# Performance work log

Hardware: AMD Instinct MI355X
Metric: run time of the kernel (lower is better)

The kernel has to match this reference:

```python
import jax, jax.numpy as jnp
import numpy as np

N = 100000   # n_node
D = 100      # emb_size
K = 100      # K1 (channel 0 cluster count)
L = 3        # layers
NNZ = 1600000  # sparse adjacency nnz (avg degree 16)


def _l2norm(x):
    # F.normalize(x, dim=-1, p=2) with eps=1e-12
    return x / jnp.maximum(jnp.linalg.norm(x, axis=-1, keepdims=True), 1e-12)


def setup_inputs() -> dict:
    key = jax.random.key(0)
    ks = jax.random.split(key, 8)
    s = 1.0 / np.sqrt(D)  # module's uniform(-stdv, stdv) init
    embedding = jax.random.normal(ks[0], (N, D), jnp.float32)
    adj = jax.random.uniform(ks[1], (N,), jnp.float32) + 0.01  # per-node positive weights
    edge_rows = jax.random.randint(ks[2], (NNZ,), 0, N, jnp.int32)
    edge_cols = jax.random.randint(ks[3], (NNZ,), 0, N, jnp.int32)
    edge_vals = jax.random.uniform(ks[4], (NNZ,), jnp.float32)
    W_item = jax.random.uniform(ks[5], (L, D, D), jnp.float32, -s, s)
    W_i1 = jax.random.uniform(ks[6], (D, D), jnp.float32, -s, s)
    W_i2 = jax.random.uniform(ks[7], (D, K), jnp.float32, -s, s)
    return {"embedding": embedding, "adj": adj, "edge_vals": edge_vals,
            "W_item": W_item, "W_i1": W_i1, "W_i2": W_i2,
            "edge_rows": edge_rows, "edge_cols": edge_cols}


def reference(embedding, adj, edge_vals, W_item, W_i1, W_i2, edge_rows, edge_cols):
    # ItemConv.forward for one channel (channel=0), adjacency as COO sparse [N,N]
    def spmm(x):  # torch.sparse.mm(adjacency, x)
        return jax.ops.segment_sum(edge_vals[:, None] * x[edge_cols], edge_rows,
                                   num_segments=N)

    x = embedding
    final = [x]
    finalh = []
    for i in range(L):
        x = x @ W_item[i]                       # Linear(D, D, bias=False)
        x = spmm(x)                             # [N, D]
        H1 = jax.nn.relu(x @ W_i1 + x)          # residual + ReLU
        H1 = jax.nn.softmax(H1 @ W_i2, axis=1)  # [N, K] soft cluster assignment
        h = H1.T * adj[None, :]                 # [K, N]
        h = h / jnp.sum(h, axis=0)              # column-normalize over clusters
        h = h @ x                               # [K, D] cluster aggregates
        h = H1 @ h                              # [N, D] redistribute to nodes
        x = h + x                               # residual
        final.append(_l2norm(x))
        finalh.append(_l2norm(h))
    item_embeddings = sum(final) / (L + 1)
    hs = sum(finalh) / L
    return item_embeddings, hs
```

## Files before the change

### kernel.cpp

```cpp
#include <hip/hip_runtime.h>
#include <hip/hip_bf16.h>

#define D 100
#define XS 128

typedef __hip_bfloat16 bf16;
typedef __attribute__((ext_vector_type(8))) short bf16x8;
typedef __attribute__((ext_vector_type(4))) float f32x4;

__device__ __forceinline__ float ldf(const void* p, long long i, int f32) {
    return f32 ? ((const float*)p)[i] : __bfloat162float(((const bf16*)p)[i]);
}

__device__ __forceinline__ float b2f(unsigned short u) {
    return __uint_as_float(((unsigned int)u) << 16);
}

__device__ __forceinline__ unsigned short f2bu(float x) {
    union { bf16 b; unsigned short u; } cv;
    cv.b = __float2bfloat16(x);
    return cv.u;
}

__global__ void detectk(const void* __restrict__ emb, int* __restrict__ flag)
{
    const unsigned short* u = (const unsigned short*)emb;
    __shared__ int cnt;
    if (threadIdx.x == 0) cnt = 0;
    __syncthreads();
    int good = 0;
    for (int i = threadIdx.x; i < 512; i += 256) {
        int e = (u[i] >> 7) & 0xFF;
        if (e >= 118 && e <= 137) good++;
    }
    atomicAdd(&cnt, good);
    __syncthreads();
    if (threadIdx.x == 0) *flag = (cnt >= 410) ? 0 : 1;
}


__global__ void wprep(const void* __restrict__ wi, const void* __restrict__ w1,
    const void* __restrict__ w2, const int* __restrict__ flag,
    bf16* __restrict__ wh, bf16* __restrict__ wl)
{
    int i = blockIdx.x * 256 + threadIdx.x;
    if (i >= 5 * 112 * 128) return;
    int m = i / (112 * 128), rem = i - m * (112 * 128);
    int c = rem / 128, k = rem - c * 128;
    float w = 0.f;
    if (c < D && k < D) {
        int f = *flag;
        long long si = (long long)k * D + c;
        if (m < 3)       w = ldf(wi, m * 10000 + si, f);
        else if (m == 3) w = ldf(w1, si, f);
        else             w = ldf(w2, si, f);
    }
    bf16 hb = __float2bfloat16(w);
    wh[i] = hb;
    wl[i] = __float2bfloat16(w - __bfloat162float(hb));
}


__global__ void hsm_conv(const float* __restrict__ hsm, bf16* __restrict__ hh,
    bf16* __restrict__ hl)
{
    int i = blockIdx.x * 256 + threadIdx.x;
    if (i >= 112 * 128) return;
    int c = i / 128, k = i - c * 128;
    float w = (c < D && k < D) ? hsm[k * D + c] : 0.f;
    bf16 hb = __float2bfloat16(w);
    hh[i] = hb;
    hl[i] = __float2bfloat16(w - __bfloat162float(hb));
}

__global__ void initk(const void* __restrict__ emb, const int* __restrict__ flag,
    bf16* __restrict__ x, float* __restrict__ o0, float* __restrict__ o1, int n)
{
    long long i = (long long)blockIdx.x * 256 + threadIdx.x;
    if (i >= (long long)n * XS) return;
    int nn = (int)(i >> 7), d = (int)(i & 127);
    float v = 0.f;
    if (d < D) v = ldf(emb, (long long)nn * D + d, *flag);
    x[i] = __float2bfloat16(v);
    if (d < D) {
        o0[(long long)nn * D + d] = v;
        o1[(long long)nn * D + d] = 0.0f;
    }
}

__global__ void fink(float* __restrict__ o0, float* __restrict__ o1, int nd)
{
    int i = blockIdx.x * 256 + threadIdx.x;
    if (i < nd) {
        o0[i] *= 0.25f;
        o1[i] *= (1.0f / 3.0f);
    }
}


template<int MODE>
__global__ __launch_bounds__(256) void gemm_mfma(
    const bf16* __restrict__ X, const bf16* __restrict__ Wh,
    const bf16* __restrict__ Wl, bf16* __restrict__ Y, int n,
    const bf16* __restrict__ X2, float* __restrict__ o0, float* __restrict__ o1)
{
    const int wave = threadIdx.x >> 6;
    const int lane = threadIdx.x & 63;
    const int r16 = lane & 15, kg = lane >> 4;
    const long long m0 = ((long long)blockIdx.x * 4 + wave) * 32;

    f32x4 acc[2][7];
    #pragma unroll
    for (int i = 0; i < 2; ++i)
        #pragma unroll
        for (int j = 0; j < 7; ++j) acc[i][j] = (f32x4){0.f, 0.f, 0.f, 0.f};

    const bf16* xa = X + (m0 + r16) * XS + kg * 8;
    #pragma unroll
    for (int ks = 0; ks < 4; ++ks) {
        bf16x8 a0 = *(const bf16x8*)(xa + ks * 32);
        bf16x8 a1 = *(const bf16x8*)(xa + 16 * XS + ks * 32);
        #pragma unroll
        for (int nt = 0; nt < 7; ++nt) {
            const bf16* wb = Wh + (nt * 16 + r16) * 128 + ks * 32 + kg * 8;
            bf16x8 bh = *(const bf16x8*)wb;
            bf16x8 bl = *(const bf16x8*)(wb + (Wl - Wh));
            acc[0][nt] = __builtin_amdgcn_mfma_f32_16x16x32_bf16(a0, bh, acc[0][nt], 0, 0, 0);
            acc[0][nt] = __builtin_amdgcn_mfma_f32_16x16x32_bf16(a0, bl, acc[0][nt], 0, 0, 0);
            acc[1][nt] = __builtin_amdgcn_mfma_f32_16x16x32_bf16(a1, bh, acc[1][nt], 0, 0, 0);
            acc[1][nt] = __builtin_amdgcn_mfma_f32_16x16x32_bf16(a1, bl, acc[1][nt], 0, 0, 0);
        }
    }

    if (MODE == 0 || MODE == 1) {
        #pragma unroll
        for (int rt = 0; rt < 2; ++rt)
            #pragma unroll
            for (int nt = 0; nt < 7; ++nt) {
                int col = nt * 16 + r16;
                #pragma unroll
                for (int r = 0; r < 4; ++r) {
                    long long row = m0 + rt * 16 + kg * 4 + r;
                    if (row >= n) continue;
                    float v = acc[rt][nt][r];
                    if (MODE == 1) {
                        v += __bfloat162float(X[row * XS + col]);
                        v = fmaxf(v, 0.f);
                    }
                    Y[row * XS + col] = __float2bfloat16(v);
                }
            }
    } else if (MODE == 2) {
        const bool v6 = (r16 < 4);
        #pragma unroll
        for (int rt = 0; rt < 2; ++rt)
            #pragma unroll
            for (int r = 0; r < 4; ++r) {
                float m = -3.0e38f;
                #pragma unroll
                for (int nt = 0; nt < 7; ++nt)
                    if (nt < 6 || v6) m = fmaxf(m, acc[rt][nt][r]);
                m = fmaxf(m, __shfl_xor(m, 1));
                m = fmaxf(m, __shfl_xor(m, 2));
                m = fmaxf(m, __shfl_xor(m, 4));
                m = fmaxf(m, __shfl_xor(m, 8));
                float ex[7]; float s = 0.f;
                #pragma unroll
                for (int nt = 0; nt < 7; ++nt) {
                    ex[nt] = (nt < 6 || v6) ? __expf(acc[rt][nt][r] - m) : 0.f;
                    s += ex[nt];
                }
                s += __shfl_xor(s, 1);
                s += __shfl_xor(s, 2);
                s += __shfl_xor(s, 4);
                s += __shfl_xor(s, 8);
                float inv = 1.f / s;
                long long row = m0 + rt * 16 + kg * 4 + r;
                if (row < n) {
                    #pragma unroll
                    for (int nt = 0; nt < 7; ++nt)
                        Y[row * XS + nt * 16 + r16] = __float2bfloat16(ex[nt] * inv);
                }
            }
    } else {
        #pragma unroll
        for (int rt = 0; rt < 2; ++rt)
            #pragma unroll
            for (int r = 0; r < 4; ++r) {
                long long row = m0 + rt * 16 + kg * 4 + r;
                float xn[7], hn[7];
                float sx = 0.f, sh2 = 0.f;
                #pragma unroll
                for (int nt = 0; nt < 7; ++nt) {
                    int col = nt * 16 + r16;
                    float h = acc[rt][nt][r];
                    float x2v = __bfloat162float(X2[row * XS + col]);
                    float xv = h + x2v;
                    xn[nt] = xv; hn[nt] = h;
                    sx += xv * xv; sh2 += h * h;
                }
                sx  += __shfl_xor(sx, 1);  sx  += __shfl_xor(sx, 2);
                sx  += __shfl_xor(sx, 4);  sx  += __shfl_xor(sx, 8);
                sh2 += __shfl_xor(sh2, 1); sh2 += __shfl_xor(sh2, 2);
                sh2 += __shfl_xor(sh2, 4); sh2 += __shfl_xor(sh2, 8);
                float ia = 1.f / fmaxf(sqrtf(sx), 1e-12f);
                float ib = 1.f / fmaxf(sqrtf(sh2), 1e-12f);
                if (row < n) {
                    long long bo = row * D;
                    #pragma unroll
                    for (int nt = 0; nt < 7; ++nt) {
                        int col = nt * 16 + r16;
                        Y[row * XS + col] = __float2bfloat16(xn[nt]);
                        if (col < D) {
                            o0[bo + col] += xn[nt] * ia;
                            o1[bo + col] += hn[nt] * ib;
                        }
                    }
                }
            }
    }

    {
        int rr = lane >> 1, half = lane & 1;
        long long row = m0 + rr;
        if (row < n)
            *(int4*)(Y + row * XS + 112 + half * 8) = make_int4(0, 0, 0, 0);
    }
}


__global__ void hist(const int* __restrict__ rows, const int* __restrict__ cols,
    int* __restrict__ cnt, int n, int nnz)
{
    int e = blockIdx.x * 256 + threadIdx.x;
    if (e >= nnz) return;
    int r = rows[e], c = cols[e];
    if ((unsigned)r >= (unsigned)n || (unsigned)c >= (unsigned)n) return;
    atomicAdd(&cnt[r], 1);
}

__global__ void scan1(const int* __restrict__ cnt, int* __restrict__ offs,
    int* __restrict__ bsum, int n)
{
    __shared__ int sh[256];
    int b = blockIdx.x, t = threadIdx.x;
    int base = b * 2048 + t * 8;
    int v[8];
    int s = 0;
    #pragma unroll
    for (int i = 0; i < 8; ++i) {
        int idx = base + i;
        v[i] = (idx < n) ? cnt[idx] : 0;
        s += v[i];
    }
    sh[t] = s; __syncthreads();
    for (int off = 1; off < 256; off <<= 1) {
        int x = (t >= off) ? sh[t - off] : 0;
        __syncthreads();
        sh[t] += x;
        __syncthreads();
    }
    int run = sh[t] - s;
    #pragma unroll
    for (int i = 0; i < 8; ++i) {
        run += v[i];
        int idx = base + i;
        if (idx < n) offs[idx + 1] = run;
    }
    if (t == 255) bsum[b] = sh[255];
}

__global__ void scan2(int* __restrict__ bsum, int nb)
{
    __shared__ int sh[256];
    int t = threadIdx.x;
    int v = (t < nb) ? bsum[t] : 0;
    sh[t] = v; __syncthreads();
    for (int off = 1; off < 256; off <<= 1) {
        int x = (t >= off) ? sh[t - off] : 0;
        __syncthreads();
        sh[t] += x;
        __syncthreads();
    }
    if (t < nb) bsum[t] = sh[t] - v;
}

__global__ void scan3(int* __restrict__ offs, const int* __restrict__ bsum, int n)
{
    int i = blockIdx.x * 256 + threadIdx.x;
    if (i == 0) offs[0] = 0;
    if (i < n) offs[i + 1] += bsum[i >> 11];
}

__global__ void scatter(const int* __restrict__ rows, const int* __restrict__ cols,
    const void* __restrict__ vals, const int* __restrict__ flag,
    const int* __restrict__ offs, int* __restrict__ fill, int2* __restrict__ ecv,
    int n, int nnz)
{
    int e = blockIdx.x * 256 + threadIdx.x;
    if (e >= nnz) return;
    int r = rows[e], c = cols[e];
    if ((unsigned)r >= (unsigned)n || (unsigned)c >= (unsigned)n) return;
    int pos = offs[r] + atomicAdd(&fill[r], 1);
    float v = ldf(vals, e, *flag);
    ecv[pos] = make_int2(c, __float_as_int(v));
}


__global__ void spmm_csr(const int* __restrict__ offs, const int2* __restrict__ ecv,
    const bf16* __restrict__ X, bf16* __restrict__ Y, int n)
{
    int wid = (int)(((long long)blockIdx.x * 256 + threadIdx.x) >> 6);
    int lane = threadIdx.x & 63;
    if (wid >= n) return;
    int s = offs[wid], e = offs[wid + 1];
    int d0 = lane * 2;
    if (d0 >= D) return;
    float a0 = 0.f, a1 = 0.f;
    int j = s;
    for (; j + 3 < e; j += 4) {
        int2 cv0 = ecv[j];
        int2 cv1 = ecv[j + 1];
        int2 cv2 = ecv[j + 2];
        int2 cv3 = ecv[j + 3];
        unsigned int u0 = *(const unsigned int*)(X + (long long)cv0.x * XS + d0);
        unsigned int u1 = *(const unsigned int*)(X + (long long)cv1.x * XS + d0);
        unsigned int u2 = *(const unsigned int*)(X + (long long)cv2.x * XS + d0);
        unsigned int u3 = *(const unsigned int*)(X + (long long)cv3.x * XS + d0);
        float v0 = __int_as_float(cv0.y), v1 = __int_as_float(cv1.y);
        float v2 = __int_as_float(cv2.y), v3 = __int_as_float(cv3.y);
        a0 = fmaf(v0, b2f((unsigned short)u0), a0);
        a1 = fmaf(v0, b2f((unsigned short)(u0 >> 16)), a1);
        a0 = fmaf(v1, b2f((unsigned short)u1), a0);
        a1 = fmaf(v1, b2f((unsigned short)(u1 >> 16)), a1);
        a0 = fmaf(v2, b2f((unsigned short)u2), a0);
        a1 = fmaf(v2, b2f((unsigned short)(u2 >> 16)), a1);
        a0 = fmaf(v3, b2f((unsigned short)u3), a0);
        a1 = fmaf(v3, b2f((unsigned short)(u3 >> 16)), a1);
    }
    for (; j < e; ++j) {
        int2 cv = ecv[j];
        unsigned int u = *(const unsigned int*)(X + (long long)cv.x * XS + d0);
        float v = __int_as_float(cv.y);
        a0 = fmaf(v, b2f((unsigned short)u), a0);
        a1 = fmaf(v, b2f((unsigned short)(u >> 16)), a1);
    }
    *(unsigned int*)(Y + (long long)wid * XS + d0) =
        ((unsigned int)f2bu(a1) << 16) | f2bu(a0);
}


#define HSM_G 250
#define HSM_BATCH 32

__global__ void hsm_partial(const bf16* __restrict__ H1, const bf16* __restrict__ X2,
    float* __restrict__ partials, int n)
{
    __shared__ float sh[HSM_BATCH][D];
    __shared__ float sx[HSM_BATCH][D];
    const int t = threadIdx.x;
    const int tk = t / 10;
    const int td = t - tk * 10;

    float acc[4][10];
    #pragma unroll
    for (int i = 0; i < 4; ++i)
        #pragma unroll
        for (int j = 0; j < 10; ++j) acc[i][j] = 0.f;

    const int per = (n + HSM_G - 1) / HSM_G;
    const int s = blockIdx.x * per;
    int e = s + per; if (e > n) e = n;

    for (int base = s; base < e; base += HSM_BATCH) {
        int cnt = e - base; if (cnt > HSM_BATCH) cnt = HSM_BATCH;
        __syncthreads();
        for (int v = t; v < cnt * 25; v += 256) {
            int r = v / 25, c4 = v - (v / 25) * 25;
            ushort4 h4 = *(const ushort4*)(H1 + (long long)(base + r) * XS + 4 * c4);
            ushort4 x4 = *(const ushort4*)(X2 + (long long)(base + r) * XS + 4 * c4);
            sh[r][4 * c4 + 0] = b2f(h4.x);
            sh[r][4 * c4 + 1] = b2f(h4.y);
            sh[r][4 * c4 + 2] = b2f(h4.z);
            sh[r][4 * c4 + 3] = b2f(h4.w);
            sx[r][4 * c4 + 0] = b2f(x4.x);
            sx[r][4 * c4 + 1] = b2f(x4.y);
            sx[r][4 * c4 + 2] = b2f(x4.z);
            sx[r][4 * c4 + 3] = b2f(x4.w);
        }
        __syncthreads();
        if (t < 250) {
            #pragma unroll 8
            for (int r = 0; r < cnt; ++r) {
                float4 a = *(const float4*)&sh[r][tk * 4];
                float b[10];
                #pragma unroll
                for (int j = 0; j < 10; ++j) b[j] = sx[r][td * 10 + j];
                #pragma unroll
                for (int j = 0; j < 10; ++j) {
                    acc[0][j] = fmaf(a.x, b[j], acc[0][j]);
                    acc[1][j] = fmaf(a.y, b[j], acc[1][j]);
                    acc[2][j] = fmaf(a.z, b[j], acc[2][j]);
                    acc[3][j] = fmaf(a.w, b[j], acc[3][j]);
                }
            }
        }
    }

    if (t < 250) {
        float* out = partials + (long long)blockIdx.x * (D * D);
        #pragma unroll
        for (int i = 0; i < 4; ++i)
            #pragma unroll
            for (int j = 0; j < 10; ++j)
                out[(tk * 4 + i) * D + td * 10 + j] = acc[i][j];
    }
}

__global__ void hsm_reduce(const float* __restrict__ partials, float* __restrict__ hsm)
{
    int i = blockIdx.x * 256 + threadIdx.x;
    if (i >= D * D) return;
    float s0 = 0.f, s1 = 0.f;
    for (int b = 0; b < HSM_G; b += 2) {
        s0 += partials[(long long)b * (D * D) + i];
        s1 += partials[(long long)(b + 1) * (D * D) + i];
    }
    hsm[i] = s0 + s1;
}


extern "C" void kernel_launch(void* const* d_in, const int* in_sizes, int n_in,
                              void* d_out, int out_size, void* d_ws, size_t ws_size,
                              hipStream_t stream)
{
    const void* emb   = d_in[0];
    const void* evals = d_in[2];
    const void* Wit   = d_in[3];
    const void* Wi1   = d_in[4];
    const void* Wi2   = d_in[5];
    const int* erows  = (const int*)d_in[6];
    const int* ecols  = (const int*)d_in[7];
    const int N   = in_sizes[0] / D;
    const int NNZ = in_sizes[2];
    const long long ND = (long long)N * D;
    const size_t NB = (size_t)N * XS * 2;

    float* o0 = (float*)d_out;
    float* o1 = o0 + ND;

    char* base = (char*)d_ws;
    size_t off = 0;
    auto alloc = [&](size_t bytes) -> void* {
        void* r = base + off;
        off += (bytes + 255) & ~(size_t)255;
        return r;
    };
    int*   flag  = (int*)  alloc(256);
    float* hsm   = (float*)alloc(D * D * 4);
    bf16*  WH    = (bf16*) alloc(5 * 112 * 128 * 2);
    bf16*  WL    = (bf16*) alloc(5 * 112 * 128 * 2);
    bf16*  hsmTh = (bf16*) alloc(112 * 128 * 2);
    bf16*  hsmTl = (bf16*) alloc(112 * 128 * 2);
    int*   offs  = (int*)  alloc(((size_t)N + 1) * 4);
    int*   cnt   = (int*)  alloc((size_t)N * 4);
    int*   bsum  = (int*)  alloc(1024);
    int2*  ecv   = (int2*) alloc((size_t)NNZ * 8);
    bf16*  B1    = (bf16*) alloc(NB);
    bf16*  B2    = (bf16*) alloc(NB);
    bf16*  H1    = (bf16*) alloc(NB);
    float* partials = (float*)alloc((size_t)HSM_G * D * D * 4);

    const int gND = (int)((ND + 255) / 256);
    const int gNX = (int)(((long long)N * XS + 255) / 256);
    const int gE  = (NNZ + 255) / 256;
    const int nb  = (N + 2047) / 2048;
    const int gM  = (N + 127) / 128;
    const int gS  = (N + 3) / 4;

    detectk<<<1, 256, 0, stream>>>(emb, flag);
    wprep<<<(5 * 112 * 128 + 255) / 256, 256, 0, stream>>>(Wit, Wi1, Wi2, flag, WH, WL);
    initk<<<gNX, 256, 0, stream>>>(emb, flag, B1, o0, o1, N);

    hipMemsetAsync(cnt, 0, (size_t)N * 4, stream);
    hist<<<gE, 256, 0, stream>>>(erows, ecols, cnt, N, NNZ);
    scan1<<<nb, 256, 0, stream>>>(cnt, offs, bsum, N);
    scan2<<<1, 256, 0, stream>>>(bsum, nb);
    scan3<<<(N + 255) / 256, 256, 0, stream>>>(offs, bsum, N);
    hipMemsetAsync(cnt, 0, (size_t)N * 4, stream);
    scatter<<<gE, 256, 0, stream>>>(erows, ecols, evals, flag, offs, cnt, ecv, N, NNZ);

    for (int l = 0; l < 3; ++l) {
        gemm_mfma<0><<<gM, 256, 0, stream>>>(B1, WH + l * 14336, WL + l * 14336,
                                             B2, N, nullptr, nullptr, nullptr);
        spmm_csr<<<gS, 256, 0, stream>>>(offs, ecv, B2, B1, N);
        gemm_mfma<1><<<gM, 256, 0, stream>>>(B1, WH + 3 * 14336, WL + 3 * 14336,
                                             B2, N, nullptr, nullptr, nullptr);
        gemm_mfma<2><<<gM, 256, 0, stream>>>(B2, WH + 4 * 14336, WL + 4 * 14336,
                                             H1, N, nullptr, nullptr, nullptr);
        hsm_partial<<<HSM_G, 256, 0, stream>>>(H1, B1, partials, N);
        hsm_reduce<<<(D * D + 255) / 256, 256, 0, stream>>>(partials, hsm);
        hsm_conv<<<(112 * 128 + 255) / 256, 256, 0, stream>>>(hsm, hsmTh, hsmTl);
        gemm_mfma<3><<<gM, 256, 0, stream>>>(H1, hsmTh, hsmTl, B1, N, B1, o0, o1);
    }
    fink<<<gND, 256, 0, stream>>>(o0, o1, (int)ND);
}
```

Measured before the change: 1.389 ms.

## Fold output scaling into epilogues, retile GEMM to one wave, deepen SpMM unroll

Several independent changes. The final scaling kernel is removed by folding the 1/4 and 1/3 factors into the init store and the GEMM epilogue. The MFMA GEMM becomes one 64-thread wave per block covering 64 rows (four row tiles), so weight loads are reused across more rows but more registers are used per thread. The SpMM inner loop is unrolled to 8 gathers for more memory-level parallelism. The hsm partials now use more blocks, read shared memory as float2 vectors, and reuse the B2 buffer instead of a separate allocation, which depends on B2 being dead at that point and large enough.

```diff
diff --git a/kernel.cpp b/kernel.cpp
--- a/kernel.cpp
+++ b/kernel.cpp
@@ -83,35 +83,25 @@
     if (d < D) v = ldf(emb, (long long)nn * D + d, *flag);
     x[i] = __float2bfloat16(v);
     if (d < D) {
-        o0[(long long)nn * D + d] = v;
+        o0[(long long)nn * D + d] = v * 0.25f;
         o1[(long long)nn * D + d] = 0.0f;
     }
 }
 
-__global__ void fink(float* __restrict__ o0, float* __restrict__ o1, int nd)
-{
-    int i = blockIdx.x * 256 + threadIdx.x;
-    if (i < nd) {
-        o0[i] *= 0.25f;
-        o1[i] *= (1.0f / 3.0f);
-    }
-}
-
 
 template<int MODE>
-__global__ __launch_bounds__(256) void gemm_mfma(
+__global__ __launch_bounds__(64) void gemm_mfma(
     const bf16* __restrict__ X, const bf16* __restrict__ Wh,
     const bf16* __restrict__ Wl, bf16* __restrict__ Y, int n,
     const bf16* __restrict__ X2, float* __restrict__ o0, float* __restrict__ o1)
 {
-    const int wave = threadIdx.x >> 6;
-    const int lane = threadIdx.x & 63;
+    const int lane = threadIdx.x;
     const int r16 = lane & 15, kg = lane >> 4;
-    const long long m0 = ((long long)blockIdx.x * 4 + wave) * 32;
-
-    f32x4 acc[2][7];
+    const long long m0 = (long long)blockIdx.x * 64;
+
+    f32x4 acc[4][7];
     #pragma unroll
-    for (int i = 0; i < 2; ++i)
+    for (int i = 0; i < 4; ++i)
         #pragma unroll
         for (int j = 0; j < 7; ++j) acc[i][j] = (f32x4){0.f, 0.f, 0.f, 0.f};
 
@@ -120,6 +110,8 @@
     for (int ks = 0; ks < 4; ++ks) {
         bf16x8 a0 = *(const bf16x8*)(xa + ks * 32);
         bf16x8 a1 = *(const bf16x8*)(xa + 16 * XS + ks * 32);
+        bf16x8 a2 = *(const bf16x8*)(xa + 32 * XS + ks * 32);
+        bf16x8 a3 = *(const bf16x8*)(xa + 48 * XS + ks * 32);
         #pragma unroll
         for (int nt = 0; nt < 7; ++nt) {
             const bf16* wb = Wh + (nt * 16 + r16) * 128 + ks * 32 + kg * 8;
@@ -129,12 +121,16 @@
             acc[0][nt] = __builtin_amdgcn_mfma_f32_16x16x32_bf16(a0, bl, acc[0][nt], 0, 0, 0);
             acc[1][nt] = __builtin_amdgcn_mfma_f32_16x16x32_bf16(a1, bh, acc[1][nt], 0, 0, 0);
             acc[1][nt] = __builtin_amdgcn_mfma_f32_16x16x32_bf16(a1, bl, acc[1][nt], 0, 0, 0);
+            acc[2][nt] = __builtin_amdgcn_mfma_f32_16x16x32_bf16(a2, bh, acc[2][nt], 0, 0, 0);
+            acc[2][nt] = __builtin_amdgcn_mfma_f32_16x16x32_bf16(a2, bl, acc[2][nt], 0, 0, 0);
+            acc[3][nt] = __builtin_amdgcn_mfma_f32_16x16x32_bf16(a3, bh, acc[3][nt], 0, 0, 0);
+            acc[3][nt] = __builtin_amdgcn_mfma_f32_16x16x32_bf16(a3, bl, acc[3][nt], 0, 0, 0);
         }
     }
 
     if (MODE == 0 || MODE == 1) {
         #pragma unroll
-        for (int rt = 0; rt < 2; ++rt)
+        for (int rt = 0; rt < 4; ++rt)
             #pragma unroll
             for (int nt = 0; nt < 7; ++nt) {
                 int col = nt * 16 + r16;
@@ -153,7 +149,7 @@
     } else if (MODE == 2) {
         const bool v6 = (r16 < 4);
         #pragma unroll
-        for (int rt = 0; rt < 2; ++rt)
+        for (int rt = 0; rt < 4; ++rt)
             #pragma unroll
             for (int r = 0; r < 4; ++r) {
                 float m = -3.0e38f;
@@ -184,7 +180,7 @@
             }
     } else {
         #pragma unroll
-        for (int rt = 0; rt < 2; ++rt)
+        for (int rt = 0; rt < 4; ++rt)
             #pragma unroll
             for (int r = 0; r < 4; ++r) {
                 long long row = m0 + rt * 16 + kg * 4 + r;
@@ -203,8 +199,8 @@
                 sx  += __shfl_xor(sx, 4);  sx  += __shfl_xor(sx, 8);
                 sh2 += __shfl_xor(sh2, 1); sh2 += __shfl_xor(sh2, 2);
                 sh2 += __shfl_xor(sh2, 4); sh2 += __shfl_xor(sh2, 8);
-                float ia = 1.f / fmaxf(sqrtf(sx), 1e-12f);
-                float ib = 1.f / fmaxf(sqrtf(sh2), 1e-12f);
+                float ia = 0.25f        / fmaxf(sqrtf(sx), 1e-12f);
+                float ib = (1.f / 3.f)  / fmaxf(sqrtf(sh2), 1e-12f);
                 if (row < n) {
                     long long bo = row * D;
                     #pragma unroll
@@ -221,10 +217,11 @@
     }
 
     {
-        int rr = lane >> 1, half = lane & 1;
-        long long row = m0 + rr;
-        if (row < n)
-            *(int4*)(Y + row * XS + 112 + half * 8) = make_int4(0, 0, 0, 0);
+        long long row = m0 + lane;
+        if (row < n) {
+            *(int4*)(Y + row * XS + 112) = make_int4(0, 0, 0, 0);
+            *(int4*)(Y + row * XS + 120) = make_int4(0, 0, 0, 0);
+        }
     }
 }
 
@@ -318,25 +315,20 @@
     if (d0 >= D) return;
     float a0 = 0.f, a1 = 0.f;
     int j = s;
-    for (; j + 3 < e; j += 4) {
-        int2 cv0 = ecv[j];
-        int2 cv1 = ecv[j + 1];
-        int2 cv2 = ecv[j + 2];
-        int2 cv3 = ecv[j + 3];
-        unsigned int u0 = *(const unsigned int*)(X + (long long)cv0.x * XS + d0);
-        unsigned int u1 = *(const unsigned int*)(X + (long long)cv1.x * XS + d0);
-        unsigned int u2 = *(const unsigned int*)(X + (long long)cv2.x * XS + d0);
-        unsigned int u3 = *(const unsigned int*)(X + (long long)cv3.x * XS + d0);
-        float v0 = __int_as_float(cv0.y), v1 = __int_as_float(cv1.y);
-        float v2 = __int_as_float(cv2.y), v3 = __int_as_float(cv3.y);
-        a0 = fmaf(v0, b2f((unsigned short)u0), a0);
-        a1 = fmaf(v0, b2f((unsigned short)(u0 >> 16)), a1);
-        a0 = fmaf(v1, b2f((unsigned short)u1), a0);
-        a1 = fmaf(v1, b2f((unsigned short)(u1 >> 16)), a1);
-        a0 = fmaf(v2, b2f((unsigned short)u2), a0);
-        a1 = fmaf(v2, b2f((unsigned short)(u2 >> 16)), a1);
-        a0 = fmaf(v3, b2f((unsigned short)u3), a0);
-        a1 = fmaf(v3, b2f((unsigned short)(u3 >> 16)), a1);
+    for (; j + 7 < e; j += 8) {
+        int2 cv[8];
+        unsigned int u[8];
+        #pragma unroll
+        for (int q = 0; q < 8; ++q) cv[q] = ecv[j + q];
+        #pragma unroll
+        for (int q = 0; q < 8; ++q)
+            u[q] = *(const unsigned int*)(X + (long long)cv[q].x * XS + d0);
+        #pragma unroll
+        for (int q = 0; q < 8; ++q) {
+            float v = __int_as_float(cv[q].y);
+            a0 = fmaf(v, b2f((unsigned short)u[q]), a0);
+            a1 = fmaf(v, b2f((unsigned short)(u[q] >> 16)), a1);
+        }
     }
     for (; j < e; ++j) {
         int2 cv = ecv[j];
@@ -350,7 +342,7 @@
 }
 
 
-#define HSM_G 250
+#define HSM_G 512
 #define HSM_BATCH 32
 
 __global__ void hsm_partial(const bf16* __restrict__ H1, const bf16* __restrict__ X2,
@@ -393,9 +385,9 @@
             #pragma unroll 8
             for (int r = 0; r < cnt; ++r) {
                 float4 a = *(const float4*)&sh[r][tk * 4];
-                float b[10];
-                #pragma unroll
-                for (int j = 0; j < 10; ++j) b[j] = sx[r][td * 10 + j];
+                const float2* bp = (const float2*)&sx[r][td * 10];
+                float2 b0 = bp[0], b1 = bp[1], b2 = bp[2], b3 = bp[3], b4 = bp[4];
+                float b[10] = {b0.x, b0.y, b1.x, b1.y, b2.x, b2.y, b3.x, b3.y, b4.x, b4.y};
                 #pragma unroll
                 for (int j = 0; j < 10; ++j) {
                     acc[0][j] = fmaf(a.x, b[j], acc[0][j]);
@@ -469,13 +461,14 @@
     bf16*  B1    = (bf16*) alloc(NB);
     bf16*  B2    = (bf16*) alloc(NB);
     bf16*  H1    = (bf16*) alloc(NB);
-    float* partials = (float*)alloc((size_t)HSM_G * D * D * 4);
+    (void)alloc(64 * XS * 2);
+    float* partials = (float*)B2;
 
     const int gND = (int)((ND + 255) / 256);
     const int gNX = (int)(((long long)N * XS + 255) / 256);
     const int gE  = (NNZ + 255) / 256;
     const int nb  = (N + 2047) / 2048;
-    const int gM  = (N + 127) / 128;
+    const int gM  = (N + 63) / 64;
     const int gS  = (N + 3) / 4;
 
     detectk<<<1, 256, 0, stream>>>(emb, flag);
@@ -491,17 +484,16 @@
     scatter<<<gE, 256, 0, stream>>>(erows, ecols, evals, flag, offs, cnt, ecv, N, NNZ);
 
     for (int l = 0; l < 3; ++l) {
-        gemm_mfma<0><<<gM, 256, 0, stream>>>(B1, WH + l * 14336, WL + l * 14336,
-                                             B2, N, nullptr, nullptr, nullptr);
+        gemm_mfma<0><<<gM, 64, 0, stream>>>(B1, WH + l * 14336, WL + l * 14336,
+                                            B2, N, nullptr, nullptr, nullptr);
         spmm_csr<<<gS, 256, 0, stream>>>(offs, ecv, B2, B1, N);
-        gemm_mfma<1><<<gM, 256, 0, stream>>>(B1, WH + 3 * 14336, WL + 3 * 14336,
-                                             B2, N, nullptr, nullptr, nullptr);
-        gemm_mfma<2><<<gM, 256, 0, stream>>>(B2, WH + 4 * 14336, WL + 4 * 14336,
-                                             H1, N, nullptr, nullptr, nullptr);
+        gemm_mfma<1><<<gM, 64, 0, stream>>>(B1, WH + 3 * 14336, WL + 3 * 14336,
+                                            B2, N, nullptr, nullptr, nullptr);
+        gemm_mfma<2><<<gM, 64, 0, stream>>>(B2, WH + 4 * 14336, WL + 4 * 14336,
+                                            H1, N, nullptr, nullptr, nullptr);
         hsm_partial<<<HSM_G, 256, 0, stream>>>(H1, B1, partials, N);
         hsm_reduce<<<(D * D + 255) / 256, 256, 0, stream>>>(partials, hsm);
         hsm_conv<<<(112 * 128 + 255) / 256, 256, 0, stream>>>(hsm, hsmTh, hsmTl);
-        gemm_mfma<3><<<gM, 256, 0, stream>>>(H1, hsmTh, hsmTl, B1, N, B1, o0, o1);
-    }
-    fink<<<gND, 256, 0, stream>>>(o0, o1, (int)ND);
-}
+        gemm_mfma<3><<<gM, 64, 0, stream>>>(H1, hsmTh, hsmTl, B1, N, B1, o0, o1);
+    }
+}
```

Result: faster. 1.279 ms (-7.9%).
